# Performance work log

Measured on AMD Instinct MI355X. Metric: run time of the kernel, lower is better.

The kernel has to match this reference:

```python
import jax, jax.numpy as jnp
import numpy as np

N_NODES = 100000
N_EDGES = 1250000
D_IN = 64
D_OUT = 64


def setup_inputs() -> dict:
    key = jax.random.key(0)
    k_h, k_e, k_src, k_dst, k_w, k_b = jax.random.split(key, 6)
    h = jax.random.normal(k_h, (N_NODES, D_IN), dtype=jnp.float32)
    e = jax.random.normal(k_e, (N_EDGES, 1), dtype=jnp.float32)
    src = jax.random.randint(k_src, (N_EDGES,), 0, N_NODES, dtype=jnp.int64)
    dst = jax.random.randint(k_dst, (N_EDGES,), 0, N_NODES, dtype=jnp.int64)
    W = jax.random.normal(k_w, (D_OUT, D_IN), dtype=jnp.float32) / np.sqrt(D_IN)
    b = jax.random.normal(k_b, (D_OUT,), dtype=jnp.float32) * 0.01
    return {"h": h, "e": e, "src": src, "dst": dst, "W": W, "b": b}


def reference(h, e, src, dst, W, b):
    # u_mul_e: gather source node features and multiply by edge features [E,1] -> [E,D]
    m = h[src] * e
    # fn.sum('m','ft'): scatter-add messages into destination nodes -> [N,D]
    ft = jax.ops.segment_sum(m, dst, num_segments=N_NODES)
    # nn.Linear(input_dim, output_dim)
    return ft @ W.T + b
```

## Files before the change

kernel.cpp:

```cpp
#include <hip/hip_runtime.h>

#define N_NODES 100000
#define N_EDGES 1250000
#define D 64
#define BUCKET_BITS 6
#define BUCKET_SZ 64
#define NBUCK 1563
#define CAP 1024
#define EPT 16
#define EPB (EPT * 256)
#define BIN_BLOCKS ((N_EDGES + EPB - 1) / EPB)
#define TR_BLOCKS ((N_NODES + 63) / 64)
#define FUSED_BLOCKS (TR_BLOCKS + BIN_BLOCKS)


typedef __attribute__((ext_vector_type(8))) short bf16x8;
typedef __attribute__((ext_vector_type(4))) float f32x4;

__device__ __forceinline__ unsigned bf16_rne(float x) {
    unsigned u = __float_as_uint(x);
    return (u + 0x7FFFu + ((u >> 16) & 1u)) >> 16;
}
__device__ __forceinline__ float bf16_to_f(unsigned short v) {
    return __uint_as_float(((unsigned)v) << 16);
}

__device__ __forceinline__ void bf16_split(float x, short& hi, short& lo) {
    unsigned hb = bf16_rne(x);
    float fh = __uint_as_float(hb << 16);
    hi = (short)hb;
    lo = (short)bf16_rne(x - fh);
}

__global__ __launch_bounds__(256) void transform_bin_kernel(const float* __restrict__ h,
                                                            const float* __restrict__ W,
                                                            unsigned short* __restrict__ g16,
                                                            const int* __restrict__ src,
                                                            const int* __restrict__ dst,
                                                            const float* __restrict__ e,
                                                            int* __restrict__ gcursor,
                                                            int2* __restrict__ packed) {
    __shared__ __align__(16) char smem_raw[12544];

    int t = threadIdx.x;
    int bx = blockIdx.x;

    if (bx < BIN_BLOCKS) {
        int* lhist = (int*)smem_raw;
        int* lcur  = lhist + NBUCK;
        int base = bx * EPB;

        for (int j = t; j < NBUCK; j += 256) { lhist[j] = 0; lcur[j] = 0; }
        __syncthreads();

#pragma unroll 8
        for (int j = 0; j < EPT; ++j) {
            int i = base + j * 256 + t;
            if (i < N_EDGES) atomicAdd(&lhist[dst[i] >> BUCKET_BITS], 1);
        }
        __syncthreads();

        for (int x = t; x < NBUCK; x += 256) {
            int c = lhist[x];
            lhist[x] = (c > 0) ? atomicAdd(&gcursor[x], c) : 0;
        }
        __syncthreads();

#pragma unroll 8
        for (int j = 0; j < EPT; ++j) {
            int i = base + j * 256 + t;
            if (i < N_EDGES) {
                int d = dst[i];
                int bk = d >> BUCKET_BITS;
                int pos = lhist[bk] + atomicAdd(&lcur[bk], 1);
                if (pos < CAP)
                    packed[bk * CAP + pos] = make_int2(src[i] | ((d & (BUCKET_SZ - 1)) << 20),
                                                       __float_as_int(e[i]));
            }
        }
    } else {
        unsigned short* sh = (unsigned short*)smem_raw;
        int trb = bx - BIN_BLOCKS;
        int lane = t & 63;
        int w = t >> 6;
        int li = lane & 15;
        int lg = lane >> 4;
        int nodebase = trb * 64 + w * 16;

        int arow = nodebase + li;
        if (arow > N_NODES - 1) arow = N_NODES - 1;

        f32x4 acc[4];
#pragma unroll
        for (int nt = 0; nt < 4; ++nt) acc[nt] = (f32x4){0.f, 0.f, 0.f, 0.f};

#pragma unroll
        for (int kk = 0; kk < 2; ++kk) {
            const float* hp = h + (long)arow * D + kk * 32 + lg * 8;
            float4 h0 = *(const float4*)hp;
            float4 h1 = *(const float4*)(hp + 4);
            float av[8] = {h0.x, h0.y, h0.z, h0.w, h1.x, h1.y, h1.z, h1.w};
            bf16x8 ahi, alo;
#pragma unroll
            for (int q = 0; q < 8; ++q) { short a, b; bf16_split(av[q], a, b); ahi[q] = a; alo[q] = b; }

#pragma unroll
            for (int nt = 0; nt < 4; ++nt) {
                const float* wp = W + (nt * 16 + li) * D + kk * 32 + lg * 8;
                float4 w0 = *(const float4*)wp;
                float4 w1 = *(const float4*)(wp + 4);
                float bv[8] = {w0.x, w0.y, w0.z, w0.w, w1.x, w1.y, w1.z, w1.w};
                bf16x8 bhi, blo;
#pragma unroll
                for (int q = 0; q < 8; ++q) { short a, b; bf16_split(bv[q], a, b); bhi[q] = a; blo[q] = b; }

                acc[nt] = __builtin_amdgcn_mfma_f32_16x16x32_bf16(ahi, bhi, acc[nt], 0, 0, 0);
                acc[nt] = __builtin_amdgcn_mfma_f32_16x16x32_bf16(ahi, blo, acc[nt], 0, 0, 0);
                acc[nt] = __builtin_amdgcn_mfma_f32_16x16x32_bf16(alo, bhi, acc[nt], 0, 0, 0);
            }
        }

#pragma unroll
        for (int nt = 0; nt < 4; ++nt) {
#pragma unroll
            for (int r = 0; r < 4; ++r) {
                sh[(w * 16 + lg * 4 + r) * D + nt * 16 + li] = (unsigned short)bf16_rne(acc[nt][r]);
            }
        }
        __syncthreads();

        const uint4* s4 = (const uint4*)sh;
        uint4* g4 = (uint4*)(g16 + (long)trb * 64 * D);
#pragma unroll
        for (int i = t; i < 512; i += 256) {
            int n = trb * 64 + (i >> 3);
            if (n < N_NODES) g4[i] = s4[i];
        }
    }
}

__global__ __launch_bounds__(512) void gather_bucket_kernel(const unsigned short* __restrict__ g16,
                                                            const int2* __restrict__ packed,
                                                            const int* __restrict__ gcursor,
                                                            const float* __restrict__ bias,
                                                            float* __restrict__ out) {
    __shared__ int2 eds[CAP];
    __shared__ int nhist[BUCKET_SZ];
    __shared__ int nbase[BUCKET_SZ];
    __shared__ int ncur[BUCKET_SZ];

    int t = threadIdx.x;
    int bk = blockIdx.x;
    int start = bk * CAP;
    int cnt = gcursor[bk];
    if (cnt > CAP) cnt = CAP;

    if (t < BUCKET_SZ) nhist[t] = 0;
    __syncthreads();

    int2 pa = make_int2(0, 0), pb = pa;
    bool va = t < cnt, vb = t + 512 < cnt;
    if (va) pa = packed[start + t];
    if (vb) pb = packed[start + t + 512];
    if (va) atomicAdd(&nhist[(pa.x >> 20) & (BUCKET_SZ - 1)], 1);
    if (vb) atomicAdd(&nhist[(pb.x >> 20) & (BUCKET_SZ - 1)], 1);
    __syncthreads();

    if (t < BUCKET_SZ) {
        int c = nhist[t];
        int v = c;
#pragma unroll
        for (int off = 1; off < BUCKET_SZ; off <<= 1) {
            int x = __shfl_up(v, off, 64);
            if (t >= off) v += x;
        }
        nbase[t] = v - c;
        ncur[t] = v - c;
    }
    __syncthreads();

    if (va) { int dl = (pa.x >> 20) & (BUCKET_SZ - 1); eds[atomicAdd(&ncur[dl], 1)] = pa; }
    if (vb) { int dl = (pb.x >> 20) & (BUCKET_SZ - 1); eds[atomicAdd(&ncur[dl], 1)] = pb; }
    __syncthreads();

    int w = t >> 6;
    int lane = t & 63;
    float bv = bias[lane];
    for (int jj = 0; jj < 8; ++jj) {
        int n = w * 8 + jj;
        int gn = bk * BUCKET_SZ + n;
        int s = nbase[n];
        int c = nhist[n];
        float acc = bv;
        int k = 0;
        for (; k + 8 <= c; k += 8) {
            int2 q0 = eds[s + k + 0], q1 = eds[s + k + 1];
            int2 q2 = eds[s + k + 2], q3 = eds[s + k + 3];
            int2 q4 = eds[s + k + 4], q5 = eds[s + k + 5];
            int2 q6 = eds[s + k + 6], q7 = eds[s + k + 7];
            float g0 = bf16_to_f(g16[(long)(q0.x & 0xFFFFF) * D + lane]);
            float g1 = bf16_to_f(g16[(long)(q1.x & 0xFFFFF) * D + lane]);
            float g2 = bf16_to_f(g16[(long)(q2.x & 0xFFFFF) * D + lane]);
            float g3 = bf16_to_f(g16[(long)(q3.x & 0xFFFFF) * D + lane]);
            float g4 = bf16_to_f(g16[(long)(q4.x & 0xFFFFF) * D + lane]);
            float g5 = bf16_to_f(g16[(long)(q5.x & 0xFFFFF) * D + lane]);
            float g6 = bf16_to_f(g16[(long)(q6.x & 0xFFFFF) * D + lane]);
            float g7 = bf16_to_f(g16[(long)(q7.x & 0xFFFFF) * D + lane]);
            acc += __int_as_float(q0.y) * g0;
            acc += __int_as_float(q1.y) * g1;
            acc += __int_as_float(q2.y) * g2;
            acc += __int_as_float(q3.y) * g3;
            acc += __int_as_float(q4.y) * g4;
            acc += __int_as_float(q5.y) * g5;
            acc += __int_as_float(q6.y) * g6;
            acc += __int_as_float(q7.y) * g7;
        }
        if (k + 4 <= c) {
            int2 q0 = eds[s + k + 0], q1 = eds[s + k + 1];
            int2 q2 = eds[s + k + 2], q3 = eds[s + k + 3];
            float g0 = bf16_to_f(g16[(long)(q0.x & 0xFFFFF) * D + lane]);
            float g1 = bf16_to_f(g16[(long)(q1.x & 0xFFFFF) * D + lane]);
            float g2 = bf16_to_f(g16[(long)(q2.x & 0xFFFFF) * D + lane]);
            float g3 = bf16_to_f(g16[(long)(q3.x & 0xFFFFF) * D + lane]);
            acc += __int_as_float(q0.y) * g0;
            acc += __int_as_float(q1.y) * g1;
            acc += __int_as_float(q2.y) * g2;
            acc += __int_as_float(q3.y) * g3;
            k += 4;
        }
        for (; k < c; ++k) {
            int2 q = eds[s + k];
            acc += __int_as_float(q.y) * bf16_to_f(g16[(long)(q.x & 0xFFFFF) * D + lane]);
        }
        if (gn < N_NODES) out[(long)gn * D + lane] = acc;
    }
}

extern "C" void kernel_launch(void* const* d_in, const int* in_sizes, int n_in,
                              void* d_out, int out_size, void* d_ws, size_t ws_size,
                              hipStream_t stream) {
    const float* h   = (const float*)d_in[0];
    const float* e   = (const float*)d_in[1];
    const int*   src = (const int*)d_in[2];
    const int*   dst = (const int*)d_in[3];
    const float* W   = (const float*)d_in[4];
    const float* b   = (const float*)d_in[5];
    float* out = (float*)d_out;

    char* ws = (char*)d_ws;
    int2*           packed  = (int2*)          (ws);
    int*            gcursor = (int*)           (ws + 12804096);
    unsigned short* g16     = (unsigned short*)(ws + 12810368);

    hipMemsetAsync(gcursor, 0, NBUCK * sizeof(int), stream);

    transform_bin_kernel<<<FUSED_BLOCKS, 256, 0, stream>>>(h, W, g16, src, dst, e, gcursor, packed);

    gather_bucket_kernel<<<NBUCK, 512, 0, stream>>>(g16, packed, gcursor, b, out);
}
```

Before: 158.1 us.

## Split fused transform/bin kernel, fold cursor reset into transform, register-cache edges

Breaks the fused transform+binning kernel into two separate kernels. The gcursor reset moves into the transform kernel, replacing the memset launch. The binning kernel now loads each edge once into registers and reuses the local atomic return value as its intra-block rank, which removes the second dst/src/e read and the lcur atomic pass. EPT is halved, giving more binning blocks. The cost is an extra kernel launch boundary and the loss of overlap between the transform and binning work.

Result: slower. 165.7 us (+4.8%).

```diff
diff --git a/kernel.cpp b/kernel.cpp
--- a/kernel.cpp
+++ b/kernel.cpp
@@ -7,11 +7,10 @@
 #define BUCKET_SZ 64
 #define NBUCK 1563
 #define CAP 1024
-#define EPT 16
+#define EPT 8
 #define EPB (EPT * 256)
 #define BIN_BLOCKS ((N_EDGES + EPB - 1) / EPB)
 #define TR_BLOCKS ((N_NODES + 63) / 64)
-#define FUSED_BLOCKS (TR_BLOCKS + BIN_BLOCKS)
 
 
 typedef __attribute__((ext_vector_type(8))) short bf16x8;
@@ -32,109 +31,114 @@
     lo = (short)bf16_rne(x - fh);
 }
 
-__global__ __launch_bounds__(256) void transform_bin_kernel(const float* __restrict__ h,
-                                                            const float* __restrict__ W,
-                                                            unsigned short* __restrict__ g16,
-                                                            const int* __restrict__ src,
-                                                            const int* __restrict__ dst,
-                                                            const float* __restrict__ e,
-                                                            int* __restrict__ gcursor,
-                                                            int2* __restrict__ packed) {
-    __shared__ __align__(16) char smem_raw[12544];
+__global__ __launch_bounds__(256) void transform_kernel(const float* __restrict__ h,
+                                                        const float* __restrict__ W,
+                                                        unsigned short* __restrict__ g16,
+                                                        int* __restrict__ gcursor) {
+    __shared__ unsigned short sh[64 * D];
 
     int t = threadIdx.x;
     int bx = blockIdx.x;
-
-    if (bx < BIN_BLOCKS) {
-        int* lhist = (int*)smem_raw;
-        int* lcur  = lhist + NBUCK;
-        int base = bx * EPB;
-
-        for (int j = t; j < NBUCK; j += 256) { lhist[j] = 0; lcur[j] = 0; }
-        __syncthreads();
-
-#pragma unroll 8
-        for (int j = 0; j < EPT; ++j) {
-            int i = base + j * 256 + t;
-            if (i < N_EDGES) atomicAdd(&lhist[dst[i] >> BUCKET_BITS], 1);
-        }
-        __syncthreads();
-
-        for (int x = t; x < NBUCK; x += 256) {
-            int c = lhist[x];
-            lhist[x] = (c > 0) ? atomicAdd(&gcursor[x], c) : 0;
-        }
-        __syncthreads();
-
-#pragma unroll 8
-        for (int j = 0; j < EPT; ++j) {
-            int i = base + j * 256 + t;
-            if (i < N_EDGES) {
-                int d = dst[i];
-                int bk = d >> BUCKET_BITS;
-                int pos = lhist[bk] + atomicAdd(&lcur[bk], 1);
-                if (pos < CAP)
-                    packed[bk * CAP + pos] = make_int2(src[i] | ((d & (BUCKET_SZ - 1)) << 20),
-                                                       __float_as_int(e[i]));
-            }
-        }
-    } else {
-        unsigned short* sh = (unsigned short*)smem_raw;
-        int trb = bx - BIN_BLOCKS;
-        int lane = t & 63;
-        int w = t >> 6;
-        int li = lane & 15;
-        int lg = lane >> 4;
-        int nodebase = trb * 64 + w * 16;
-
-        int arow = nodebase + li;
-        if (arow > N_NODES - 1) arow = N_NODES - 1;
-
-        f32x4 acc[4];
-#pragma unroll
-        for (int nt = 0; nt < 4; ++nt) acc[nt] = (f32x4){0.f, 0.f, 0.f, 0.f};
-
-#pragma unroll
-        for (int kk = 0; kk < 2; ++kk) {
-            const float* hp = h + (long)arow * D + kk * 32 + lg * 8;
-            float4 h0 = *(const float4*)hp;
-            float4 h1 = *(const float4*)(hp + 4);
-            float av[8] = {h0.x, h0.y, h0.z, h0.w, h1.x, h1.y, h1.z, h1.w};
-            bf16x8 ahi, alo;
-#pragma unroll
-            for (int q = 0; q < 8; ++q) { short a, b; bf16_split(av[q], a, b); ahi[q] = a; alo[q] = b; }
-
-#pragma unroll
-            for (int nt = 0; nt < 4; ++nt) {
-                const float* wp = W + (nt * 16 + li) * D + kk * 32 + lg * 8;
-                float4 w0 = *(const float4*)wp;
-                float4 w1 = *(const float4*)(wp + 4);
-                float bv[8] = {w0.x, w0.y, w0.z, w0.w, w1.x, w1.y, w1.z, w1.w};
-                bf16x8 bhi, blo;
-#pragma unroll
-                for (int q = 0; q < 8; ++q) { short a, b; bf16_split(bv[q], a, b); bhi[q] = a; blo[q] = b; }
-
-                acc[nt] = __builtin_amdgcn_mfma_f32_16x16x32_bf16(ahi, bhi, acc[nt], 0, 0, 0);
-                acc[nt] = __builtin_amdgcn_mfma_f32_16x16x32_bf16(ahi, blo, acc[nt], 0, 0, 0);
-                acc[nt] = __builtin_amdgcn_mfma_f32_16x16x32_bf16(alo, bhi, acc[nt], 0, 0, 0);
-            }
-        }
+    if (bx < 7) {
+        int i = bx * 256 + t;
+        if (i < NBUCK) gcursor[i] = 0;
+    }
+
+    int lane = t & 63;
+    int w = t >> 6;
+    int li = lane & 15;
+    int lg = lane >> 4;
+    int nodebase = bx * 64 + w * 16;
+
+    int arow = nodebase + li;
+    if (arow > N_NODES - 1) arow = N_NODES - 1;
+
+    f32x4 acc[4];
+#pragma unroll
+    for (int nt = 0; nt < 4; ++nt) acc[nt] = (f32x4){0.f, 0.f, 0.f, 0.f};
+
+#pragma unroll
+    for (int kk = 0; kk < 2; ++kk) {
+        const float* hp = h + (long)arow * D + kk * 32 + lg * 8;
+        float4 h0 = *(const float4*)hp;
+        float4 h1 = *(const float4*)(hp + 4);
+        float av[8] = {h0.x, h0.y, h0.z, h0.w, h1.x, h1.y, h1.z, h1.w};
+        bf16x8 ahi, alo;
+#pragma unroll
+        for (int q = 0; q < 8; ++q) { short a, b; bf16_split(av[q], a, b); ahi[q] = a; alo[q] = b; }
 
 #pragma unroll
         for (int nt = 0; nt < 4; ++nt) {
-#pragma unroll
-            for (int r = 0; r < 4; ++r) {
-                sh[(w * 16 + lg * 4 + r) * D + nt * 16 + li] = (unsigned short)bf16_rne(acc[nt][r]);
-            }
-        }
-        __syncthreads();
-
-        const uint4* s4 = (const uint4*)sh;
-        uint4* g4 = (uint4*)(g16 + (long)trb * 64 * D);
-#pragma unroll
-        for (int i = t; i < 512; i += 256) {
-            int n = trb * 64 + (i >> 3);
-            if (n < N_NODES) g4[i] = s4[i];
+            const float* wp = W + (nt * 16 + li) * D + kk * 32 + lg * 8;
+            float4 w0 = *(const float4*)wp;
+            float4 w1 = *(const float4*)(wp + 4);
+            float bv[8] = {w0.x, w0.y, w0.z, w0.w, w1.x, w1.y, w1.z, w1.w};
+            bf16x8 bhi, blo;
+#pragma unroll
+            for (int q = 0; q < 8; ++q) { short a, b; bf16_split(bv[q], a, b); bhi[q] = a; blo[q] = b; }
+
+            acc[nt] = __builtin_amdgcn_mfma_f32_16x16x32_bf16(ahi, bhi, acc[nt], 0, 0, 0);
+            acc[nt] = __builtin_amdgcn_mfma_f32_16x16x32_bf16(ahi, blo, acc[nt], 0, 0, 0);
+            acc[nt] = __builtin_amdgcn_mfma_f32_16x16x32_bf16(alo, bhi, acc[nt], 0, 0, 0);
+        }
+    }
+
+#pragma unroll
+    for (int nt = 0; nt < 4; ++nt) {
+#pragma unroll
+        for (int r = 0; r < 4; ++r) {
+            sh[(w * 16 + lg * 4 + r) * D + nt * 16 + li] = (unsigned short)bf16_rne(acc[nt][r]);
+        }
+    }
+    __syncthreads();
+
+    const uint4* s4 = (const uint4*)sh;
+    uint4* g4 = (uint4*)(g16 + (long)bx * 64 * D);
+#pragma unroll
+    for (int i = t; i < 512; i += 256) {
+        int n = bx * 64 + (i >> 3);
+        if (n < N_NODES) g4[i] = s4[i];
+    }
+}
+
+__global__ __launch_bounds__(256) void bin_edges_kernel(const int* __restrict__ src,
+                                                        const int* __restrict__ dst,
+                                                        const float* __restrict__ e,
+                                                        int* __restrict__ gcursor,
+                                                        int2* __restrict__ packed) {
+    __shared__ int lhist[NBUCK];
+    int t = threadIdx.x;
+    for (int j = t; j < NBUCK; j += 256) lhist[j] = 0;
+    __syncthreads();
+
+    int b[EPT], r[EPT], sv[EPT];
+    float ev[EPT];
+    int base = blockIdx.x * EPB;
+#pragma unroll
+    for (int j = 0; j < EPT; ++j) {
+        int i = base + j * 256 + t;
+        b[j] = -1;
+        if (i < N_EDGES) {
+            int d = dst[i];
+            b[j] = d >> BUCKET_BITS;
+            sv[j] = src[i] | ((d & (BUCKET_SZ - 1)) << 20);
+            ev[j] = e[i];
+            r[j] = atomicAdd(&lhist[b[j]], 1);
+        }
+    }
+    __syncthreads();
+
+    for (int x = t; x < NBUCK; x += 256) {
+        int c = lhist[x];
+        lhist[x] = (c > 0) ? atomicAdd(&gcursor[x], c) : 0;
+    }
+    __syncthreads();
+
+#pragma unroll
+    for (int j = 0; j < EPT; ++j) {
+        if (b[j] >= 0) {
+            int pos = lhist[b[j]] + r[j];
+            if (pos < CAP) packed[b[j] * CAP + pos] = make_int2(sv[j], __float_as_int(ev[j]));
         }
     }
 }
@@ -252,9 +256,9 @@
     int*            gcursor = (int*)           (ws + 12804096);
     unsigned short* g16     = (unsigned short*)(ws + 12810368);
 
-    hipMemsetAsync(gcursor, 0, NBUCK * sizeof(int), stream);
-
-    transform_bin_kernel<<<FUSED_BLOCKS, 256, 0, stream>>>(h, W, g16, src, dst, e, gcursor, packed);
+    transform_kernel<<<TR_BLOCKS, 256, 0, stream>>>(h, W, g16, gcursor);
+
+    bin_edges_kernel<<<BIN_BLOCKS, 256, 0, stream>>>(src, dst, e, gcursor, packed);
 
     gather_bucket_kernel<<<NBUCK, 512, 0, stream>>>(g16, packed, gcursor, b, out);
 }
```
